# Performance work log

Hardware: AMD Instinct MI355X
Metric: run time of the kernel (lower is better)

Reference implementation:

```python
import jax, jax.numpy as jnp
import numpy as np

L, H, P, R = 8192, 1024, 512, 256


def setup_inputs() -> dict:
    key = jax.random.key(0)
    ks = jax.random.split(key, 12)
    nrm = lambda k, s, std=0.01: std * jax.random.normal(k, s, dtype=jnp.float32)
    # Stable complex diagonal: |Lambda_bar| in [0.8, 0.999)
    mag = 0.8 + 0.199 * jax.random.uniform(ks[8], (P,), dtype=jnp.float32)
    phase = jnp.pi * jax.random.uniform(ks[9], (P,), dtype=jnp.float32)
    return {
        "input_sequence": jax.random.normal(ks[0], (L, H), dtype=jnp.float32),
        "F": nrm(ks[1], (R, H)),
        "H_proj": nrm(ks[2], (R, H)),
        "Delta_p": jnp.eye(R, dtype=jnp.float32),
        "Delta_r": jnp.eye(R, dtype=jnp.float32),
        "E": nrm(ks[3], (P, R)),
        "G": nrm(ks[4], (H, R)),
        "Lambda_bar_re": (mag * jnp.cos(phase)).astype(jnp.float32),
        "Lambda_bar_im": (mag * jnp.sin(phase)).astype(jnp.float32),
        "B_bar_re": nrm(ks[5], (P, H), 0.05),
        "B_bar_im": nrm(ks[6], (P, H), 0.05),
        "C_re": nrm(ks[7], (H, P), 0.05),
        "C_im": nrm(ks[10], (H, P), 0.05),
        "D": nrm(ks[11], (H, H), 0.02),
    }


def _binop(a, b):
    # Diagonal linear SSM associative combine: (lam, bu)
    return (b[0] * a[0], b[0] * a[1] + b[1])


def reference(input_sequence, F, H_proj, Delta_p, Delta_r, E, G,
              Lambda_bar_re, Lambda_bar_im, B_bar_re, B_bar_im,
              C_re, C_im, D):
    # p_k = Delta_p @ (F @ u_k), r_k = Delta_r @ (H_proj @ u_k)  -- vmapped over L via matmul
    p_seq = (input_sequence @ F.T) @ Delta_p.T            # (L, R)
    r_seq = (input_sequence @ H_proj.T) @ Delta_r.T       # (L, R)
    up_seq = jnp.concatenate([input_sequence, p_seq], axis=-1)  # (L, H+R)

    Lam = (Lambda_bar_re + 1j * Lambda_bar_im).astype(jnp.complex64)         # (P,)
    B_bar = (B_bar_re + 1j * B_bar_im).astype(jnp.complex64)                 # (P, H)
    B_ext = jnp.concatenate([B_bar, E.astype(jnp.complex64)], axis=1)        # (P, H+R)

    # Per-step driving term Bu_k = B_ext @ up_k
    Bu = up_seq.astype(jnp.complex64) @ B_ext.T                               # (L, P)
    Lam_el = jnp.broadcast_to(Lam, Bu.shape)                                  # (L, P)

    # Parallel associative scan: x_k = Lam * x_{k-1} + Bu_k
    _, xs = jax.lax.associative_scan(_binop, (Lam_el, Bu))                    # (L, P)

    C_tilde = (C_re + 1j * C_im).astype(jnp.complex64)                        # (H, P)
    # conj_sym=True branch: y_k = 2*Re(C_tilde @ x_k) + G @ r_k + D @ u_k
    y_seq = (2.0 * jnp.real(xs @ C_tilde.T)
             + r_seq @ G.T
             + input_sequence @ D.T)                                           # (L, H)
    return y_seq
```

## Files before the change

### kernel.cpp

```cpp
#include <hip/hip_runtime.h>
#include <stdint.h>

#define L_SEQ 8192
#define NCHUNK 64
#define CHUNK  128

typedef __attribute__((ext_vector_type(8))) short bf16x8;
typedef __attribute__((ext_vector_type(4))) float f32x4;

__device__ inline unsigned short f2bf(float x) {
  unsigned u = __builtin_bit_cast(unsigned, x);
  unsigned r = (u + 0x7fffu + ((u >> 16) & 1u)) >> 16;
  return (unsigned short)r;
}

#define GLD16(g, l)                                                            \
  __builtin_amdgcn_global_load_lds(                                            \
      (const __attribute__((address_space(1))) unsigned int*)(g),              \
      (__attribute__((address_space(3))) unsigned int*)(l), 16, 0, 0)

__global__ __launch_bounds__(256) void prep(
    const float* __restrict__ F, const float* __restrict__ Hp,
    const float* __restrict__ dP, const float* __restrict__ dR,
    const float* __restrict__ E, const float* __restrict__ G,
    const float* __restrict__ Bim, const float* __restrict__ Cre,
    const float* __restrict__ Cim, const float* __restrict__ u,
    unsigned short* __restrict__ Ft, unsigned short* __restrict__ Ht,
    unsigned short* __restrict__ dPb, unsigned short* __restrict__ dRb,
    unsigned short* __restrict__ Eb, unsigned short* __restrict__ Gb,
    unsigned short* __restrict__ W1im, unsigned short* __restrict__ Wy,
    unsigned short* __restrict__ A2) {
  int q = blockIdx.x * 256 + threadIdx.x;
  if (q < 65536) {
    int e = q * 4, i = e >> 8, j = e & 255;
    ushort4 o;
    o.x = f2bf(F[(size_t)(j + 0) * 1024 + i]);
    o.y = f2bf(F[(size_t)(j + 1) * 1024 + i]);
    o.z = f2bf(F[(size_t)(j + 2) * 1024 + i]);
    o.w = f2bf(F[(size_t)(j + 3) * 1024 + i]);
    *(ushort4*)(Ft + e) = o;
  } else if (q < 131072) {
    int e = (q - 65536) * 4, i = e >> 8, j = e & 255;
    ushort4 o;
    o.x = f2bf(Hp[(size_t)(j + 0) * 1024 + i]);
    o.y = f2bf(Hp[(size_t)(j + 1) * 1024 + i]);
    o.z = f2bf(Hp[(size_t)(j + 2) * 1024 + i]);
    o.w = f2bf(Hp[(size_t)(j + 3) * 1024 + i]);
    *(ushort4*)(Ht + e) = o;
  } else if (q < 147456) {
    int e = (q - 131072) * 4;
    float4 v = *(const float4*)(dP + e);
    ushort4 o = {f2bf(v.x), f2bf(v.y), f2bf(v.z), f2bf(v.w)};
    *(ushort4*)(dPb + e) = o;
  } else if (q < 163840) {
    int e = (q - 147456) * 4;
    float4 v = *(const float4*)(dR + e);
    ushort4 o = {f2bf(v.x), f2bf(v.y), f2bf(v.z), f2bf(v.w)};
    *(ushort4*)(dRb + e) = o;
  } else if (q < 196608) {
    int e = (q - 163840) * 4;
    float4 v = *(const float4*)(E + e);
    ushort4 o = {f2bf(v.x), f2bf(v.y), f2bf(v.z), f2bf(v.w)};
    *(ushort4*)(Eb + e) = o;
  } else if (q < 262144) {
    int e = (q - 196608) * 4;
    float4 v = *(const float4*)(G + e);
    ushort4 o = {f2bf(v.x), f2bf(v.y), f2bf(v.z), f2bf(v.w)};
    *(ushort4*)(Gb + e) = o;
  } else if (q < 393216) {
    int e = (q - 262144) * 4;
    float4 v = *(const float4*)(Bim + e);
    ushort4 o = {f2bf(v.x), f2bf(v.y), f2bf(v.z), f2bf(v.w)};
    *(ushort4*)(W1im + e) = o;
  } else if (q < 524288) {
    int e = (q - 393216) * 4, i = e >> 9, j = e & 511;
    float4 v = *(const float4*)(Cre + (size_t)i * 512 + j);
    ushort4 o = {f2bf(2.f * v.x), f2bf(2.f * v.y), f2bf(2.f * v.z), f2bf(2.f * v.w)};
    *(ushort4*)(Wy + (size_t)i * 2048 + 1024 + j) = o;
  } else if (q < 655360) {
    int e = (q - 524288) * 4, i = e >> 9, j = e & 511;
    float4 v = *(const float4*)(Cim + (size_t)i * 512 + j);
    ushort4 o = {f2bf(-2.f * v.x), f2bf(-2.f * v.y), f2bf(-2.f * v.z), f2bf(-2.f * v.w)};
    *(ushort4*)(Wy + (size_t)i * 2048 + 1536 + j) = o;
  } else {
    int e = (q - 655360) * 4, i = e >> 10, j = e & 1023;
    float4 v = *(const float4*)(u + (size_t)i * 1024 + j);
    ushort4 o = {f2bf(v.x), f2bf(v.y), f2bf(v.z), f2bf(v.w)};
    *(ushort4*)(A2 + (size_t)i * 2048 + j) = o;
  }
}

template <int HAS_ADD, int OUT_F32, int OUT_BF16>
__device__ __forceinline__ void gemm_body(
    const unsigned short* __restrict__ A, int lda,
    const unsigned short* __restrict__ B, int ldb,
    float* __restrict__ C, int ldc,
    unsigned short* __restrict__ Cb, int ldcb,
    const float* __restrict__ Add, int ldadd, int K, int m0, int n0,
    unsigned short* sA, unsigned short* sB) {
  const int tid = threadIdx.x;
  const int lane = tid & 63, wave = tid >> 6;
  const int wm = wave >> 1, wn = wave & 1;
  const int frow = lane & 15, fg = lane >> 4;

  const int srow = lane >> 2;
  const int scol = (lane & 3) * 8;
  const unsigned short* gA0 = A + (size_t)(m0 + wave * 32 + srow) * lda + scol;
  const unsigned short* gA1 = gA0 + (size_t)16 * lda;
  const unsigned short* gB0 = B + (size_t)(n0 + wave * 32 + srow) * ldb + scol;
  const unsigned short* gB1 = gB0 + (size_t)16 * ldb;
  unsigned short* lA0 = sA + wave * 1024;
  unsigned short* lA1 = lA0 + 512;
  unsigned short* lB0 = sB + wave * 1024;
  unsigned short* lB1 = lB0 + 512;

  f32x4 acc[4][4] = {};

  for (int kt = 0; kt < K; kt += 32) {
    __syncthreads();
    GLD16(gA0 + kt, lA0);
    GLD16(gA1 + kt, lA1);
    GLD16(gB0 + kt, lB0);
    GLD16(gB1 + kt, lB1);
    __syncthreads();
    bf16x8 fa[4], fb[4];
#pragma unroll
    for (int f = 0; f < 4; ++f) {
      fa[f] = *(const bf16x8*)(sA + (wm * 64 + f * 16 + frow) * 32 + fg * 8);
      fb[f] = *(const bf16x8*)(sB + (wn * 64 + f * 16 + frow) * 32 + fg * 8);
    }
#pragma unroll
    for (int i = 0; i < 4; ++i)
#pragma unroll
      for (int j = 0; j < 4; ++j)
        acc[i][j] = __builtin_amdgcn_mfma_f32_16x16x32_bf16(fa[i], fb[j], acc[i][j], 0, 0, 0);
  }

  const int crow4 = (lane >> 4) * 4, ccol = lane & 15;
#pragma unroll
  for (int i = 0; i < 4; ++i)
#pragma unroll
    for (int j = 0; j < 4; ++j)
#pragma unroll
      for (int q = 0; q < 4; ++q) {
        int r = m0 + wm * 64 + i * 16 + crow4 + q;
        int c = n0 + wn * 64 + j * 16 + ccol;
        float v = acc[i][j][q];
        if (HAS_ADD) v += Add[(size_t)r * ldadd + c];
        if (OUT_F32) C[(size_t)r * ldc + c] = v;
        if (OUT_BF16) Cb[(size_t)r * ldcb + c] = f2bf(v);
      }
}

template <int HAS_ADD, int OUT_F32, int OUT_BF16>
__global__ __launch_bounds__(256) void gemm_bt(
    const unsigned short* __restrict__ A, int lda,
    const unsigned short* __restrict__ B, int ldb,
    float* __restrict__ C, int ldc,
    unsigned short* __restrict__ Cb, int ldcb,
    const float* __restrict__ Add, int ldadd, int K) {
  __shared__ __align__(16) unsigned short sA[128 * 32];
  __shared__ __align__(16) unsigned short sB[128 * 32];
  gemm_body<HAS_ADD, OUT_F32, OUT_BF16>(A, lda, B, ldb, C, ldc, Cb, ldcb, Add,
                                        ldadd, K, blockIdx.x * 128,
                                        blockIdx.y * 128, sA, sB);
}

struct GemmP {
  const unsigned short* A; int lda;
  const unsigned short* B; int ldb;
  float* C; int ldc;
  unsigned short* Cb; int ldcb;
  const float* Add; int ldadd;
  int K; int gx;
};

template <int HAS_ADD, int OUT_F32, int OUT_BF16>
__global__ __launch_bounds__(256) void gemm_bt_dual(GemmP p0, GemmP p1) {
  __shared__ __align__(16) unsigned short sA[128 * 32];
  __shared__ __align__(16) unsigned short sB[128 * 32];
  GemmP p = blockIdx.z ? p1 : p0;
  if ((int)blockIdx.x >= p.gx) return;
  gemm_body<HAS_ADD, OUT_F32, OUT_BF16>(p.A, p.lda, p.B, p.ldb, p.C, p.ldc,
                                        p.Cb, p.ldcb, p.Add, p.ldadd, p.K,
                                        blockIdx.x * 128, blockIdx.y * 128, sA, sB);
}

__global__ __launch_bounds__(256) void scan_carry(const float* __restrict__ Bu,
                                                  const float* __restrict__ lre,
                                                  const float* __restrict__ lim,
                                                  float2* __restrict__ carry2) {
  int g = blockIdx.x * 256 + threadIdx.x;
  int p = g & 511, c = g >> 9;
  float ar = lre[p], ai = lim[p];
  float sr = 0.f, si = 0.f;
  const float* base = Bu + (size_t)c * CHUNK * 1024 + p;
#pragma unroll 4
  for (int i = 0; i < CHUNK; ++i) {
    float br = base[(size_t)i * 1024];
    float bi = base[(size_t)i * 1024 + 512];
    float nr = ar * sr - ai * si + br;
    float ni = ar * si + ai * sr + bi;
    sr = nr; si = ni;
  }
  carry2[(size_t)p * NCHUNK + c] = make_float2(sr, si);
}

__global__ __launch_bounds__(512) void scan_prefix(const float2* __restrict__ carry2,
                                                   const float* __restrict__ lre,
                                                   const float* __restrict__ lim,
                                                   float2* __restrict__ prefix2) {
  int p = threadIdx.x;
  float ar = lre[p], ai = lim[p];
  float cr = ar, ci = ai;
#pragma unroll
  for (int s = 0; s < 7; ++s) {
    float t = cr * cr - ci * ci;
    ci = 2.f * cr * ci;
    cr = t;
  }
  float sr = 0.f, si = 0.f;
  const float2* cp = carry2 + (size_t)p * NCHUNK;
  float2* pp = prefix2 + (size_t)p * NCHUNK;
  for (int cb = 0; cb < NCHUNK; cb += 16) {
    float2 cv[16];
#pragma unroll
    for (int i = 0; i < 16; ++i) cv[i] = cp[cb + i];
#pragma unroll
    for (int i = 0; i < 16; ++i) {
      float nr = cr * sr - ci * si + cv[i].x;
      float ni = cr * si + ci * sr + cv[i].y;
      sr = nr; si = ni;
      pp[cb + i] = make_float2(sr, si);
    }
  }
}

__global__ __launch_bounds__(256) void scan_apply(const float* __restrict__ Bu,
                                                  const float* __restrict__ lre,
                                                  const float* __restrict__ lim,
                                                  const float2* __restrict__ prefix2,
                                                  unsigned short* __restrict__ A2) {
  int g = blockIdx.x * 256 + threadIdx.x;
  int p = g & 511, c = g >> 9;
  float ar = lre[p], ai = lim[p];
  float sr = 0.f, si = 0.f;
  if (c > 0) {
    float2 pr = prefix2[(size_t)p * NCHUNK + c - 1];
    sr = pr.x; si = pr.y;
  }
  const float* base = Bu + (size_t)c * CHUNK * 1024 + p;
  unsigned short* ob = A2 + (size_t)c * CHUNK * 2048 + 1024 + p;
#pragma unroll 4
  for (int i = 0; i < CHUNK; ++i) {
    float br = base[(size_t)i * 1024];
    float bi = base[(size_t)i * 1024 + 512];
    float nr = ar * sr - ai * si + br;
    float ni = ar * si + ai * sr + bi;
    sr = nr; si = ni;
    ob[(size_t)i * 2048] = f2bf(sr);
    ob[(size_t)i * 2048 + 512] = f2bf(si);
  }
}

extern "C" void kernel_launch(void* const* d_in, const int* in_sizes, int n_in,
                              void* d_out, int out_size, void* d_ws, size_t ws_size,
                              hipStream_t stream) {
  const float* u   = (const float*)d_in[0];
  const float* F   = (const float*)d_in[1];
  const float* Hp  = (const float*)d_in[2];
  const float* dP  = (const float*)d_in[3];
  const float* dR  = (const float*)d_in[4];
  const float* E   = (const float*)d_in[5];
  const float* G   = (const float*)d_in[6];
  const float* lre = (const float*)d_in[7];
  const float* lim = (const float*)d_in[8];
  const float* Bre = (const float*)d_in[9];
  const float* Bim = (const float*)d_in[10];
  const float* Cre = (const float*)d_in[11];
  const float* Cim = (const float*)d_in[12];
  const float* Dm  = (const float*)d_in[13];
  float* y = (float*)d_out;

  uint8_t* ws = (uint8_t*)d_ws;
  size_t off = 0;
  auto alloc = [&](size_t bytes) {
    void* p = ws + off;
    off += (bytes + 255) & ~(size_t)255;
    return p;
  };
  unsigned short* A2  = (unsigned short*)alloc((size_t)L_SEQ * 2048 * 2);
  unsigned short* W1  = (unsigned short*)alloc((size_t)1024 * 1024 * 2);
  unsigned short* Wy  = (unsigned short*)alloc((size_t)1024 * 2048 * 2);
  float*          Bu  = (float*)alloc((size_t)L_SEQ * 1024 * 4);
  unsigned short* Ft  = (unsigned short*)alloc((size_t)1024 * 256 * 2);
  unsigned short* Ht  = (unsigned short*)alloc((size_t)1024 * 256 * 2);
  unsigned short* FpT = (unsigned short*)alloc((size_t)1024 * 256 * 2);
  unsigned short* HrT = (unsigned short*)alloc((size_t)1024 * 256 * 2);
  unsigned short* dPb = (unsigned short*)alloc((size_t)256 * 256 * 2);
  unsigned short* dRb = (unsigned short*)alloc((size_t)256 * 256 * 2);
  unsigned short* Eb  = (unsigned short*)alloc((size_t)512 * 256 * 2);
  unsigned short* Gb  = (unsigned short*)alloc((size_t)1024 * 256 * 2);
  float* carry  = (float*)alloc((size_t)512 * NCHUNK * 8);
  float* prefix = (float*)alloc((size_t)512 * NCHUNK * 8);
  (void)ws_size; (void)in_sizes; (void)n_in; (void)out_size;

  prep<<<10752, 256, 0, stream>>>(F, Hp, dP, dR, E, G, Bim, Cre, Cim, u,
                                  Ft, Ht, dPb, dRb, Eb, Gb,
                                  W1 + (size_t)512 * 1024, Wy, A2);

  GemmP pa = {Ft, 256, dPb, 256, nullptr, 0, FpT, 256, nullptr, 0, 256, 8};
  GemmP pb = {Ht, 256, dRb, 256, nullptr, 0, HrT, 256, nullptr, 0, 256, 8};
  gemm_bt_dual<0, 0, 1><<<dim3(8, 2, 2), 256, 0, stream>>>(pa, pb);

  GemmP pc = {Eb, 256, FpT, 256, nullptr, 0, W1, 1024, Bre, 1024, 256, 4};
  GemmP pd = {Gb, 256, HrT, 256, nullptr, 0, Wy, 2048, Dm, 1024, 256, 8};
  gemm_bt_dual<1, 0, 1><<<dim3(8, 8, 2), 256, 0, stream>>>(pc, pd);

  gemm_bt<0, 1, 0><<<dim3(64, 8), 256, 0, stream>>>(A2, 2048, W1, 1024, Bu, 1024,
                                                    nullptr, 0, nullptr, 0, 1024);

  scan_carry<<<128, 256, 0, stream>>>(Bu, lre, lim, (float2*)carry);
  scan_prefix<<<1, 512, 0, stream>>>((const float2*)carry, lre, lim, (float2*)prefix);
  scan_apply<<<128, 256, 0, stream>>>(Bu, lre, lim, (const float2*)prefix, A2);

  gemm_bt<0, 1, 0><<<dim3(64, 8), 256, 0, stream>>>(A2, 2048, Wy, 2048, y, 1024,
                                                    nullptr, 0, nullptr, 0, 2048);
}
```

Measured before the change: 270.6 us.

## Double-buffer GEMM LDS, store Bu as bf16, interleave complex layout, tile transposes

The GEMM main loop now double-buffers its LDS tiles, so the next k-slice's global-to-LDS loads overlap the MFMAs on the current one. This removes one barrier per iteration at the cost of twice the shared memory. Bu is written as interleaved re/im bf16 instead of fp32, which halves the traffic of the Bu GEMM output and of both scan passes; the scans now do one 32-bit load and one 32-bit store per step. W1 and Wy rows and columns are reordered to the interleaved complex layout to match. The F/H transposes in prep now go through a shared-memory tile for coalesced access. Rounding Bu to bf16 before the long recurrence adds precision risk.

```diff
diff --git a/kernel.cpp b/kernel.cpp
--- a/kernel.cpp
+++ b/kernel.cpp
@@ -12,6 +12,10 @@
   unsigned u = __builtin_bit_cast(unsigned, x);
   unsigned r = (u + 0x7fffu + ((u >> 16) & 1u)) >> 16;
   return (unsigned short)r;
+}
+__device__ inline float bf2f(unsigned short b) {
+  unsigned u = ((unsigned)b) << 16;
+  return __builtin_bit_cast(float, u);
 }
 
 #define GLD16(g, l)                                                            \
@@ -28,62 +32,59 @@
     unsigned short* __restrict__ Ft, unsigned short* __restrict__ Ht,
     unsigned short* __restrict__ dPb, unsigned short* __restrict__ dRb,
     unsigned short* __restrict__ Eb, unsigned short* __restrict__ Gb,
-    unsigned short* __restrict__ W1im, unsigned short* __restrict__ Wy,
+    unsigned short* __restrict__ W1, unsigned short* __restrict__ Wy,
     unsigned short* __restrict__ A2) {
-  int q = blockIdx.x * 256 + threadIdx.x;
-  if (q < 65536) {
-    int e = q * 4, i = e >> 8, j = e & 255;
-    ushort4 o;
-    o.x = f2bf(F[(size_t)(j + 0) * 1024 + i]);
-    o.y = f2bf(F[(size_t)(j + 1) * 1024 + i]);
-    o.z = f2bf(F[(size_t)(j + 2) * 1024 + i]);
-    o.w = f2bf(F[(size_t)(j + 3) * 1024 + i]);
-    *(ushort4*)(Ft + e) = o;
-  } else if (q < 131072) {
-    int e = (q - 65536) * 4, i = e >> 8, j = e & 255;
-    ushort4 o;
-    o.x = f2bf(Hp[(size_t)(j + 0) * 1024 + i]);
-    o.y = f2bf(Hp[(size_t)(j + 1) * 1024 + i]);
-    o.z = f2bf(Hp[(size_t)(j + 2) * 1024 + i]);
-    o.w = f2bf(Hp[(size_t)(j + 3) * 1024 + i]);
-    *(ushort4*)(Ht + e) = o;
-  } else if (q < 147456) {
-    int e = (q - 131072) * 4;
-    float4 v = *(const float4*)(dP + e);
+  __shared__ float tile[32][33];
+  const int b = blockIdx.x, tid = threadIdx.x;
+  if (b < 512) {
+    const float* src = (b < 256) ? F : Hp;
+    unsigned short* dst = (b < 256) ? Ft : Ht;
+    int bb = b & 255;
+    int bx = bb & 31, by = bb >> 5;
+    int tx = tid & 31, ty = tid >> 5;
+#pragma unroll
+    for (int dy = 0; dy < 32; dy += 8)
+      tile[ty + dy][tx] = src[(size_t)(by * 32 + ty + dy) * 1024 + bx * 32 + tx];
+    __syncthreads();
+#pragma unroll
+    for (int dy = 0; dy < 32; dy += 8)
+      dst[(size_t)(bx * 32 + ty + dy) * 256 + by * 32 + tx] = f2bf(tile[tx][ty + dy]);
+    return;
+  }
+  if (b < 1024) {
+    const float* src;
+    unsigned short* dst;
+    int q;
+    if (b < 576)      { src = dP; dst = dPb; q = (b - 512) * 256 + tid; }
+    else if (b < 640) { src = dR; dst = dRb; q = (b - 576) * 256 + tid; }
+    else if (b < 768) { src = E;  dst = Eb;  q = (b - 640) * 256 + tid; }
+    else              { src = G;  dst = Gb;  q = (b - 768) * 256 + tid; }
+    int e = q * 4;
+    float4 v = *(const float4*)(src + e);
     ushort4 o = {f2bf(v.x), f2bf(v.y), f2bf(v.z), f2bf(v.w)};
-    *(ushort4*)(dPb + e) = o;
-  } else if (q < 163840) {
-    int e = (q - 147456) * 4;
-    float4 v = *(const float4*)(dR + e);
+    *(ushort4*)(dst + e) = o;
+    return;
+  }
+  if (b < 1536) {
+    int q = (b - 1024) * 256 + tid;
+    int e = q * 4, p = e >> 10, j = e & 1023;
+    float4 v = *(const float4*)(Bim + (size_t)p * 1024 + j);
     ushort4 o = {f2bf(v.x), f2bf(v.y), f2bf(v.z), f2bf(v.w)};
-    *(ushort4*)(dRb + e) = o;
-  } else if (q < 196608) {
-    int e = (q - 163840) * 4;
-    float4 v = *(const float4*)(E + e);
-    ushort4 o = {f2bf(v.x), f2bf(v.y), f2bf(v.z), f2bf(v.w)};
-    *(ushort4*)(Eb + e) = o;
-  } else if (q < 262144) {
-    int e = (q - 196608) * 4;
-    float4 v = *(const float4*)(G + e);
-    ushort4 o = {f2bf(v.x), f2bf(v.y), f2bf(v.z), f2bf(v.w)};
-    *(ushort4*)(Gb + e) = o;
-  } else if (q < 393216) {
-    int e = (q - 262144) * 4;
-    float4 v = *(const float4*)(Bim + e);
-    ushort4 o = {f2bf(v.x), f2bf(v.y), f2bf(v.z), f2bf(v.w)};
-    *(ushort4*)(W1im + e) = o;
-  } else if (q < 524288) {
-    int e = (q - 393216) * 4, i = e >> 9, j = e & 511;
-    float4 v = *(const float4*)(Cre + (size_t)i * 512 + j);
-    ushort4 o = {f2bf(2.f * v.x), f2bf(2.f * v.y), f2bf(2.f * v.z), f2bf(2.f * v.w)};
-    *(ushort4*)(Wy + (size_t)i * 2048 + 1024 + j) = o;
-  } else if (q < 655360) {
-    int e = (q - 524288) * 4, i = e >> 9, j = e & 511;
-    float4 v = *(const float4*)(Cim + (size_t)i * 512 + j);
-    ushort4 o = {f2bf(-2.f * v.x), f2bf(-2.f * v.y), f2bf(-2.f * v.z), f2bf(-2.f * v.w)};
-    *(ushort4*)(Wy + (size_t)i * 2048 + 1536 + j) = o;
-  } else {
-    int e = (q - 655360) * 4, i = e >> 10, j = e & 1023;
+    *(ushort4*)(W1 + (size_t)(2 * p + 1) * 1024 + j) = o;
+    return;
+  }
+  if (b < 2560) {
+    int q = (b - 1536) * 256 + tid;
+    int i = q >> 8, jp = (q & 255) * 2;
+    float2 re = *(const float2*)(Cre + (size_t)i * 512 + jp);
+    float2 im = *(const float2*)(Cim + (size_t)i * 512 + jp);
+    ushort4 o = {f2bf(2.f * re.x), f2bf(-2.f * im.x), f2bf(2.f * re.y), f2bf(-2.f * im.y)};
+    *(ushort4*)(Wy + (size_t)i * 2048 + 1024 + 2 * jp) = o;
+    return;
+  }
+  {
+    int q = (b - 2560) * 256 + tid;
+    int e = q * 4, i = e >> 10, j = e & 1023;
     float4 v = *(const float4*)(u + (size_t)i * 1024 + j);
     ushort4 o = {f2bf(v.x), f2bf(v.y), f2bf(v.z), f2bf(v.w)};
     *(ushort4*)(A2 + (size_t)i * 2048 + j) = o;
@@ -109,31 +110,42 @@
   const unsigned short* gA1 = gA0 + (size_t)16 * lda;
   const unsigned short* gB0 = B + (size_t)(n0 + wave * 32 + srow) * ldb + scol;
   const unsigned short* gB1 = gB0 + (size_t)16 * ldb;
-  unsigned short* lA0 = sA + wave * 1024;
-  unsigned short* lA1 = lA0 + 512;
-  unsigned short* lB0 = sB + wave * 1024;
-  unsigned short* lB1 = lB0 + 512;
 
   f32x4 acc[4][4] = {};
-
-  for (int kt = 0; kt < K; kt += 32) {
-    __syncthreads();
-    GLD16(gA0 + kt, lA0);
-    GLD16(gA1 + kt, lA1);
-    GLD16(gB0 + kt, lB0);
-    GLD16(gB1 + kt, lB1);
-    __syncthreads();
+  const int nt = K >> 5;
+
+  {
+    unsigned short* a0 = sA + wave * 1024;
+    unsigned short* b0 = sB + wave * 1024;
+    GLD16(gA0, a0); GLD16(gA1, a0 + 512);
+    GLD16(gB0, b0); GLD16(gB1, b0 + 512);
+  }
+  __syncthreads();
+
+  for (int t = 0; t < nt; ++t) {
+    const int cur = (t & 1) * 4096;
+    if (t + 1 < nt) {
+      const int nxt = 4096 - cur;
+      const int kt = (t + 1) * 32;
+      unsigned short* a0 = sA + nxt + wave * 1024;
+      unsigned short* b0 = sB + nxt + wave * 1024;
+      GLD16(gA0 + kt, a0); GLD16(gA1 + kt, a0 + 512);
+      GLD16(gB0 + kt, b0); GLD16(gB1 + kt, b0 + 512);
+    }
+    const unsigned short* bA = sA + cur;
+    const unsigned short* bB = sB + cur;
     bf16x8 fa[4], fb[4];
 #pragma unroll
     for (int f = 0; f < 4; ++f) {
-      fa[f] = *(const bf16x8*)(sA + (wm * 64 + f * 16 + frow) * 32 + fg * 8);
-      fb[f] = *(const bf16x8*)(sB + (wn * 64 + f * 16 + frow) * 32 + fg * 8);
+      fa[f] = *(const bf16x8*)(bA + (wm * 64 + f * 16 + frow) * 32 + fg * 8);
+      fb[f] = *(const bf16x8*)(bB + (wn * 64 + f * 16 + frow) * 32 + fg * 8);
     }
 #pragma unroll
     for (int i = 0; i < 4; ++i)
 #pragma unroll
       for (int j = 0; j < 4; ++j)
         acc[i][j] = __builtin_amdgcn_mfma_f32_16x16x32_bf16(fa[i], fb[j], acc[i][j], 0, 0, 0);
+    __syncthreads();
   }
 
   const int crow4 = (lane >> 4) * 4, ccol = lane & 15;
@@ -159,8 +171,8 @@
     float* __restrict__ C, int ldc,
     unsigned short* __restrict__ Cb, int ldcb,
     const float* __restrict__ Add, int ldadd, int K) {
-  __shared__ __align__(16) unsigned short sA[128 * 32];
-  __shared__ __align__(16) unsigned short sB[128 * 32];
+  __shared__ __align__(16) unsigned short sA[2 * 128 * 32];
+  __shared__ __align__(16) unsigned short sB[2 * 128 * 32];
   gemm_body<HAS_ADD, OUT_F32, OUT_BF16>(A, lda, B, ldb, C, ldc, Cb, ldcb, Add,
                                         ldadd, K, blockIdx.x * 128,
                                         blockIdx.y * 128, sA, sB);
@@ -177,8 +189,8 @@
 
 template <int HAS_ADD, int OUT_F32, int OUT_BF16>
 __global__ __launch_bounds__(256) void gemm_bt_dual(GemmP p0, GemmP p1) {
-  __shared__ __align__(16) unsigned short sA[128 * 32];
-  __shared__ __align__(16) unsigned short sB[128 * 32];
+  __shared__ __align__(16) unsigned short sA[2 * 128 * 32];
+  __shared__ __align__(16) unsigned short sB[2 * 128 * 32];
   GemmP p = blockIdx.z ? p1 : p0;
   if ((int)blockIdx.x >= p.gx) return;
   gemm_body<HAS_ADD, OUT_F32, OUT_BF16>(p.A, p.lda, p.B, p.ldb, p.C, p.ldc,
@@ -186,7 +198,7 @@
                                         blockIdx.x * 128, blockIdx.y * 128, sA, sB);
 }
 
-__global__ __launch_bounds__(256) void scan_carry(const float* __restrict__ Bu,
+__global__ __launch_bounds__(256) void scan_carry(const unsigned short* __restrict__ Bub,
                                                   const float* __restrict__ lre,
                                                   const float* __restrict__ lim,
                                                   float2* __restrict__ carry2) {
@@ -194,11 +206,12 @@
   int p = g & 511, c = g >> 9;
   float ar = lre[p], ai = lim[p];
   float sr = 0.f, si = 0.f;
-  const float* base = Bu + (size_t)c * CHUNK * 1024 + p;
-#pragma unroll 4
+  const unsigned short* base = Bub + (size_t)c * CHUNK * 1024 + 2 * p;
+#pragma unroll 8
   for (int i = 0; i < CHUNK; ++i) {
-    float br = base[(size_t)i * 1024];
-    float bi = base[(size_t)i * 1024 + 512];
+    unsigned w = *(const unsigned*)(base + (size_t)i * 1024);
+    float br = bf2f((unsigned short)(w & 0xffff));
+    float bi = bf2f((unsigned short)(w >> 16));
     float nr = ar * sr - ai * si + br;
     float ni = ar * si + ai * sr + bi;
     sr = nr; si = ni;
@@ -236,7 +249,7 @@
   }
 }
 
-__global__ __launch_bounds__(256) void scan_apply(const float* __restrict__ Bu,
+__global__ __launch_bounds__(256) void scan_apply(const unsigned short* __restrict__ Bub,
                                                   const float* __restrict__ lre,
                                                   const float* __restrict__ lim,
                                                   const float2* __restrict__ prefix2,
@@ -249,17 +262,17 @@
     float2 pr = prefix2[(size_t)p * NCHUNK + c - 1];
     sr = pr.x; si = pr.y;
   }
-  const float* base = Bu + (size_t)c * CHUNK * 1024 + p;
-  unsigned short* ob = A2 + (size_t)c * CHUNK * 2048 + 1024 + p;
-#pragma unroll 4
+  const unsigned short* base = Bub + (size_t)c * CHUNK * 1024 + 2 * p;
+  unsigned* ob = (unsigned*)(A2 + (size_t)c * CHUNK * 2048 + 1024 + 2 * p);
+#pragma unroll 8
   for (int i = 0; i < CHUNK; ++i) {
-    float br = base[(size_t)i * 1024];
-    float bi = base[(size_t)i * 1024 + 512];
+    unsigned w = *(const unsigned*)(base + (size_t)i * 1024);
+    float br = bf2f((unsigned short)(w & 0xffff));
+    float bi = bf2f((unsigned short)(w >> 16));
     float nr = ar * sr - ai * si + br;
     float ni = ar * si + ai * sr + bi;
     sr = nr; si = ni;
-    ob[(size_t)i * 2048] = f2bf(sr);
-    ob[(size_t)i * 2048 + 512] = f2bf(si);
+    ob[(size_t)i * 1024] = (unsigned)f2bf(sr) | ((unsigned)f2bf(si) << 16);
   }
 }
 
@@ -292,7 +305,7 @@
   unsigned short* A2  = (unsigned short*)alloc((size_t)L_SEQ * 2048 * 2);
   unsigned short* W1  = (unsigned short*)alloc((size_t)1024 * 1024 * 2);
   unsigned short* Wy  = (unsigned short*)alloc((size_t)1024 * 2048 * 2);
-  float*          Bu  = (float*)alloc((size_t)L_SEQ * 1024 * 4);
+  unsigned short* Bub = (unsigned short*)alloc((size_t)L_SEQ * 1024 * 2);
   unsigned short* Ft  = (unsigned short*)alloc((size_t)1024 * 256 * 2);
   unsigned short* Ht  = (unsigned short*)alloc((size_t)1024 * 256 * 2);
   unsigned short* FpT = (unsigned short*)alloc((size_t)1024 * 256 * 2);
@@ -306,23 +319,22 @@
   (void)ws_size; (void)in_sizes; (void)n_in; (void)out_size;
 
   prep<<<10752, 256, 0, stream>>>(F, Hp, dP, dR, E, G, Bim, Cre, Cim, u,
-                                  Ft, Ht, dPb, dRb, Eb, Gb,
-                                  W1 + (size_t)512 * 1024, Wy, A2);
+                                  Ft, Ht, dPb, dRb, Eb, Gb, W1, Wy, A2);
 
   GemmP pa = {Ft, 256, dPb, 256, nullptr, 0, FpT, 256, nullptr, 0, 256, 8};
   GemmP pb = {Ht, 256, dRb, 256, nullptr, 0, HrT, 256, nullptr, 0, 256, 8};
   gemm_bt_dual<0, 0, 1><<<dim3(8, 2, 2), 256, 0, stream>>>(pa, pb);
 
-  GemmP pc = {Eb, 256, FpT, 256, nullptr, 0, W1, 1024, Bre, 1024, 256, 4};
+  GemmP pc = {Eb, 256, FpT, 256, nullptr, 0, W1, 2048, Bre, 1024, 256, 4};
   GemmP pd = {Gb, 256, HrT, 256, nullptr, 0, Wy, 2048, Dm, 1024, 256, 8};
   gemm_bt_dual<1, 0, 1><<<dim3(8, 8, 2), 256, 0, stream>>>(pc, pd);
 
-  gemm_bt<0, 1, 0><<<dim3(64, 8), 256, 0, stream>>>(A2, 2048, W1, 1024, Bu, 1024,
-                                                    nullptr, 0, nullptr, 0, 1024);
-
-  scan_carry<<<128, 256, 0, stream>>>(Bu, lre, lim, (float2*)carry);
+  gemm_bt<0, 0, 1><<<dim3(64, 8), 256, 0, stream>>>(A2, 2048, W1, 1024, nullptr, 0,
+                                                    Bub, 1024, nullptr, 0, 1024);
+
+  scan_carry<<<128, 256, 0, stream>>>(Bub, lre, lim, (float2*)carry);
   scan_prefix<<<1, 512, 0, stream>>>((const float2*)carry, lre, lim, (float2*)prefix);
-  scan_apply<<<128, 256, 0, stream>>>(Bu, lre, lim, (const float2*)prefix, A2);
+  scan_apply<<<128, 256, 0, stream>>>(Bub, lre, lim, (const float2*)prefix, A2);
 
   gemm_bt<0, 1, 0><<<dim3(64, 8), 256, 0, stream>>>(A2, 2048, Wy, 2048, y, 1024,
                                                     nullptr, 0, nullptr, 0, 2048);
```

Result: faster. 241.0 us (-10.9%).
